# Performance work log

Hardware: AMD Instinct MI355X
Metric: run time of the kernel (lower is better)

## Reference

```python
import jax, jax.numpy as jnp
import numpy as np

K = 3
TAPS = K ** 3  # 27 taps of the 3x3x3 kernel


def _conv3d(x, w, b):
    # x: (B,C,T,H,W), w: (O,I,kT,kH,kW), stride 1, pad 1
    y = jax.lax.conv_general_dilated(
        x, w, window_strides=(1, 1, 1),
        padding=((1, 1), (1, 1), (1, 1)),
        dimension_numbers=('NCDHW', 'OIDHW', 'NCDHW'))
    return y + b[None, :, None, None, None]


def _bilinear(xt, ph, pw):
    # xt: (B,C,T,H,W) temporally-shifted features; ph/pw: (B,T,H,W) float coords
    # zero padding outside the spatial extent (matches deform-conv semantics)
    B, C, T, H, W = xt.shape
    h0 = jnp.floor(ph)
    w0 = jnp.floor(pw)
    lh = (ph - h0)[:, None]  # (B,1,T,H,W)
    lw = (pw - w0)[:, None]
    h0i = h0.astype(jnp.int32)
    w0i = w0.astype(jnp.int32)
    xf = xt.reshape(B, C, T, H * W)

    def gather(hi, wi):
        valid = (hi >= 0) & (hi < H) & (wi >= 0) & (wi < W)
        idx = (jnp.clip(hi, 0, H - 1) * W + jnp.clip(wi, 0, W - 1)).reshape(B, 1, T, H * W)
        v = jnp.take_along_axis(xf, jnp.broadcast_to(idx, (B, C, T, H * W)), axis=3)
        return v.reshape(B, C, T, H, W) * valid[:, None].astype(xt.dtype)

    v00 = gather(h0i, w0i)
    v01 = gather(h0i, w0i + 1)
    v10 = gather(h0i + 1, w0i)
    v11 = gather(h0i + 1, w0i + 1)
    return (v00 * (1 - lh) * (1 - lw) + v01 * (1 - lh) * lw
            + v10 * lh * (1 - lw) + v11 * lh * lw)


def _dcn_hw(x, w_off, b_off, w, b):
    # DeformConvPack_d with dimension='HW': offsets deform H/W only, temporal taps rigid
    B, C, T, H, W = x.shape
    off = _conv3d(x, w_off, b_off).reshape(B, TAPS, 2, T, H, W)  # (dy, dx) per tap
    x_pad = jnp.pad(x, ((0, 0), (0, 0), (1, 1), (0, 0), (0, 0)))  # zero pad T
    hh = jnp.arange(H, dtype=x.dtype)[None, None, :, None]
    ww = jnp.arange(W, dtype=x.dtype)[None, None, None, :]
    out = jnp.zeros((B, w.shape[0], T, H, W), x.dtype)
    k = 0
    for kt in range(K):
        xt = x_pad[:, :, kt:kt + T]  # rigid temporal shift for this tap
        for kh in range(K):
            for kw in range(K):
                ph = hh + (kh - 1) + off[:, k, 0]
                pw = ww + (kw - 1) + off[:, k, 1]
                s = _bilinear(xt, ph, pw)  # (B,C,T,H,W)
                out = out + jnp.einsum('bcthw,oc->bothw', s, w[:, :, kt, kh, kw])
                k += 1
    return out + b[None, :, None, None, None]


def setup_inputs() -> dict:
    key = jax.random.key(0)
    ks = jax.random.split(key, 9)
    nf, B, T, H, W = 64, 1, 7, 96, 96
    sc = 1.0 / np.sqrt(nf * TAPS)
    return {
        'x': jax.random.normal(ks[0], (B, nf, T, H, W), jnp.float32),
        'w_off0': jax.random.normal(ks[1], (2 * TAPS, nf, K, K, K), jnp.float32) * 0.01,
        'b_off0': jax.random.normal(ks[2], (2 * TAPS,), jnp.float32) * 0.01,
        'w0': jax.random.normal(ks[3], (nf, nf, K, K, K), jnp.float32) * sc,
        'b0': jax.random.normal(ks[4], (nf,), jnp.float32) * 0.01,
        'w_off1': jax.random.normal(ks[5], (2 * TAPS, nf, K, K, K), jnp.float32) * 0.01,
        'b_off1': jax.random.normal(ks[6], (2 * TAPS,), jnp.float32) * 0.01,
        'w1': jax.random.normal(ks[7], (nf, nf, K, K, K), jnp.float32) * sc,
        'b1': jax.random.normal(ks[8], (nf,), jnp.float32) * 0.01,
    }


def reference(x, w_off0, b_off0, w0, b0, w_off1, b_off1, w1, b1):
    y = _dcn_hw(x, w_off0, b_off0, w0, b0)
    y = jnp.where(y > 0, y, 0.1 * y)  # LeakyReLU(0.1)
    return _dcn_hw(y, w_off1, b_off1, w1, b1) + x
```

## Files before the change

kernel.cpp:

```cpp
#include <hip/hip_runtime.h>
#include <hip/hip_fp16.h>

#define T_DIM 7
#define H_DIM 96
#define W_DIM 96
#define HW    (H_DIM*W_DIM)
#define L_DIM (T_DIM*HW)
#define NTAPS 27

#define TR 8
#define TC 16
#define HR (TR+8)
#define HC (TC+8)
#define HROWB (HC*128)
#define HALO_B (HR*HROWB)
#define WBUF_OFF HALO_B
#define SOFF_OFF (HALO_B + 16384)
#define SOFF_STRIDE 108
#define SMEM_B (SOFF_OFF + 128*SOFF_STRIDE)

typedef __attribute__((ext_vector_type(8))) _Float16 f16x8;
typedef __attribute__((ext_vector_type(4))) float f32x4;

#define GLOAD16(gp, lp) \
    __builtin_amdgcn_global_load_lds((const __attribute__((address_space(1))) unsigned int*)(gp), \
                                     (__attribute__((address_space(3))) unsigned int*)(lp), 16, 0, 0)

__global__ void prep_weights(const float* __restrict__ woff0,
                             const float* __restrict__ w0,
                             const float* __restrict__ woff1,
                             const float* __restrict__ w1,
                             unsigned short* __restrict__ dst)
{
    int idx = blockIdx.x * 256 + threadIdx.x;
    const int per = NTAPS * 64 * 64;
    if (idx >= 4 * per) return;
    int which = idx / per;
    int r     = idx % per;
    int tap   = r / 4096;
    int o     = (r >> 6) & 63;
    int c     = r & 63;
    const float* src = (which == 0) ? woff0 : (which == 1) ? w0
                     : (which == 2) ? woff1 : w1;
    int omax = (which == 0 || which == 2) ? 54 : 64;
    float v = 0.f;
    if (o < omax) v = src[(o * 64 + c) * NTAPS + tap];
    __half h = __float2half(v);
    int slot = (((c >> 3) + o) & 7);
    int pos  = tap * 4096 + o * 64 + slot * 8 + (c & 7);
    dst[which * per + pos] = __half_as_ushort(h);
}

__global__ void transpose_x(const float* __restrict__ x, unsigned* __restrict__ xt2)
{
    __shared__ float tile[64][65];
    const int tid = threadIdx.x;
    const int lb  = blockIdx.x * 64;
    const int ln  = tid & 63;
    const int q   = tid >> 6;
#pragma unroll
    for (int i = 0; i < 16; ++i) {
        int c = q + 4 * i;
        tile[ln][c] = x[(size_t)c * L_DIM + lb + ln];
    }
    __syncthreads();
    const int ln2 = tid & 31, q2 = tid >> 5;
#pragma unroll
    for (int i = 0; i < 8; ++i) {
        int ll = q2 + 8 * i;
        __half2 h2 = __float22half2_rn(make_float2(tile[ll][2*ln2], tile[ll][2*ln2+1]));
        xt2[(size_t)(lb + ll) * 32 + ln2] = *reinterpret_cast<unsigned*>(&h2);
    }
}

#define STAGE_SLAB(KT) { \
    int tp_ = t + (KT) - 1; \
    int tps_ = min(max(tp_, 0), T_DIM - 1); \
    const unsigned char* sb_ = xb + (size_t)tps_ * HW * 128; \
    _Pragma("unroll") \
    for (int i = 0; i < 12; ++i) { \
        int p16_ = tid + i * 256; \
        int hr_ = p16_ / 192; \
        int rem_ = p16_ - hr_ * 192; \
        int hc_ = rem_ >> 3; \
        int sl_ = rem_ & 7; \
        int ch_ = (sl_ - hc_) & 7; \
        int gr_ = min(max(row0 - 4 + hr_, 0), H_DIM - 1); \
        int gc_ = min(max(col0 - 4 + hc_, 0), W_DIM - 1); \
        GLOAD16(sb_ + (size_t)(gr_ * W_DIM + gc_) * 128 + ch_ * 16, \
                smem + (i << 12) + (wv << 10)); \
    } }

#define WSTAGE(WG, K) { \
    const unsigned char* ws_ = (WG) + (size_t)(K) * 8192 + tid * 16; \
    unsigned char* ld_ = smem + WBUF_OFF + (((K) & 1) << 13) + (wv << 10); \
    GLOAD16(ws_,        ld_); \
    GLOAD16(ws_ + 4096, ld_ + 4096); }

#define READ_OFF(MT, K) ({ \
    unsigned u_ = *(const unsigned*)(smem + SOFF_OFF + \
        ((2 * wv + (MT)) * 16 + lr) * SOFF_STRIDE + (K) * 4); \
    __half22float2(*reinterpret_cast<__half2*>(&u_)); })

#define GATHER_D(MT, O2, A0, A1) { \
    float ph_ = (float)(row0 + 2 * wv + (MT) + kh - 1) + (O2).x; \
    float pw_ = (float)(col0 + lr + kw - 1) + (O2).y; \
    float hf_ = floorf(ph_), wf_ = floorf(pw_); \
    float lh_ = ph_ - hf_, lw_ = pw_ - wf_; \
    int h0_ = (int)hf_, w0_ = (int)wf_; \
    __align__(16) __half2 va_[8]; \
    const __half2 z2_ = __float2half2_rn(0.f); \
    _Pragma("unroll") \
    for (int p = 0; p < 8; ++p) va_[p] = z2_; \
    _Pragma("unroll") \
    for (int j = 0; j < 4; ++j) { \
        int hj_ = h0_ + (j >> 1), wj_ = w0_ + (j & 1); \
        bool v_ = tv && (hj_ >= 0) && (hj_ < H_DIM) && (wj_ >= 0) && (wj_ < W_DIM); \
        float wg_ = ((j >> 1) ? lh_ : 1.f - lh_) * ((j & 1) ? lw_ : 1.f - lw_); \
        __half2 cw_ = __float2half2_rn(v_ ? wg_ : 0.f); \
        int sr_ = min(max(hj_ - row0 + 4, 0), HR - 1); \
        int sc_ = min(max(wj_ - col0 + 4, 0), HC - 1); \
        const unsigned char* cell_ = smem + sr_ * HROWB + sc_ * 128; \
        f16x8 c0_ = *(const f16x8*)(cell_ + (((lk + sc_) & 7) << 4)); \
        f16x8 c1_ = *(const f16x8*)(cell_ + (((lk + 4 + sc_) & 7) << 4)); \
        const __half2* p0_ = (const __half2*)&c0_; \
        const __half2* p1_ = (const __half2*)&c1_; \
        _Pragma("unroll") \
        for (int d = 0; d < 4; ++d) { \
            va_[d]     = __hfma2(p0_[d], cw_, va_[d]); \
            va_[4 + d] = __hfma2(p1_[d], cw_, va_[4 + d]); \
        } \
    } \
    A0 = *reinterpret_cast<f16x8*>(&va_[0]); \
    A1 = *reinterpret_cast<f16x8*>(&va_[4]); }

#define GATHER_C(MT, A0, A1) { \
    int hj_ = row0 + 2 * wv + (MT) + kh - 1, wj_ = col0 + lr + kw - 1; \
    bool v_ = tv && (hj_ >= 0) && (hj_ < H_DIM) && (wj_ >= 0) && (wj_ < W_DIM); \
    int sr_ = 2 * wv + (MT) + kh + 3, sc_ = lr + kw + 3; \
    const unsigned char* cell_ = smem + sr_ * HROWB + sc_ * 128; \
    int4 z0_ = *(const int4*)(cell_ + (((lk + sc_) & 7) << 4)); \
    int4 z1_ = *(const int4*)(cell_ + (((lk + 4 + sc_) & 7) << 4)); \
    if (!v_) { z0_ = make_int4(0,0,0,0); z1_ = make_int4(0,0,0,0); } \
    A0 = *reinterpret_cast<f16x8*>(&z0_); \
    A1 = *reinterpret_cast<f16x8*>(&z1_); }

#define MFMA_F16(A, B, C) __builtin_amdgcn_mfma_f32_16x16x32_f16( \
    A, *reinterpret_cast<f16x8*>(&(B)), C, 0, 0, 0)

#define RUN_PHASE(DEF, WGBLP) { \
    const unsigned char* wgbl_ = (WGBLP); \
    asm volatile("s_waitcnt lgkmcnt(0)" ::: "memory"); \
    __builtin_amdgcn_s_barrier(); \
    STAGE_SLAB(0); \
    WSTAGE(wgbl_, 0); \
    float2 oc0, oc1, on0, on1; \
    oc0 = make_float2(0.f, 0.f); oc1 = oc0; on0 = oc0; on1 = oc0; \
    if (DEF) { oc0 = READ_OFF(0, 0); oc1 = READ_OFF(1, 0); } \
    asm volatile("s_waitcnt vmcnt(0)" ::: "memory"); \
    __builtin_amdgcn_s_barrier(); \
    __builtin_amdgcn_sched_barrier(0); \
    _Pragma("unroll 1") \
    for (int kt = 0; kt < 3; ++kt) { \
        if (kt > 0) { \
            asm volatile("s_waitcnt lgkmcnt(0)" ::: "memory"); \
            __builtin_amdgcn_s_barrier(); \
            STAGE_SLAB(kt); \
            asm volatile("s_waitcnt vmcnt(0)" ::: "memory"); \
            __builtin_amdgcn_s_barrier(); \
            __builtin_amdgcn_sched_barrier(0); \
        } \
        int tp = t + kt - 1; \
        bool tv = (tp >= 0) && (tp < T_DIM); \
        _Pragma("unroll 1") \
        for (int k9 = 0; k9 < 9; ++k9) { \
            int k = kt * 9 + k9; \
            if (k > 0) { \
                asm volatile("s_waitcnt vmcnt(0) lgkmcnt(0)" ::: "memory"); \
                __builtin_amdgcn_s_barrier(); \
                __builtin_amdgcn_sched_barrier(0); \
            } \
            if (k + 1 < NTAPS) { \
                WSTAGE(wgbl_, k + 1); \
                if (DEF) { on0 = READ_OFF(0, k + 1); on1 = READ_OFF(1, k + 1); } \
            } \
            int kh = k9 / 3, kw = k9 - (k9 / 3) * 3; \
            f16x8 a00, a01, a10, a11; \
            if (DEF) { GATHER_D(0, oc0, a00, a01); GATHER_D(1, oc1, a10, a11); } \
            else     { GATHER_C(0, a00, a01);      GATHER_C(1, a10, a11); } \
            const unsigned char* br_ = smem + WBUF_OFF + ((k & 1) << 13) + lr * 128; \
            _Pragma("unroll") \
            for (int n = 0; n < 4; ++n) { \
                f16x8 b0_ = *(const f16x8*)(br_ + n * 2048 + s0); \
                f16x8 b1_ = *(const f16x8*)(br_ + n * 2048 + s1); \
                acc[0][n] = MFMA_F16(a00, b0_, acc[0][n]); \
                acc[0][n] = MFMA_F16(a01, b1_, acc[0][n]); \
                acc[1][n] = MFMA_F16(a10, b0_, acc[1][n]); \
                acc[1][n] = MFMA_F16(a11, b1_, acc[1][n]); \
            } \
            oc0 = on0; oc1 = on1; \
        } \
    } }

template<int EPI>
__global__ __launch_bounds__(256, 2)
void dcn_m32(const unsigned short* __restrict__ xin,
             const unsigned short* __restrict__ Wtoff,
             const unsigned short* __restrict__ Wtm,
             const float* __restrict__ boff,
             const float* __restrict__ bmain,
             const float* __restrict__ resid,
             float* __restrict__ outf,
             unsigned short* __restrict__ outh)
{
    __shared__ __align__(16) unsigned char smem[SMEM_B];

    const int tid  = threadIdx.x;
    const int wv   = tid >> 6, lane = tid & 63;
    const int lr   = lane & 15, lk = lane >> 4;

    const int bid = blockIdx.x;
    const int wg  = (bid & 7) * 63 + (bid >> 3);
    const int t   = wg / 72;
    const int rg  = (wg % 72) / 6;
    const int cg  = wg % 6;
    const int row0 = rg * TR;
    const int col0 = cg * TC;

    const unsigned char* xb = (const unsigned char*)xin;

    const int s0 = ((lk + lr) & 7) << 4;
    const int s1 = ((lk + 4 + lr) & 7) << 4;

    f32x4 acc[2][4];
#pragma unroll
    for (int mt = 0; mt < 2; ++mt)
#pragma unroll
        for (int n = 0; n < 4; ++n) acc[mt][n] = (f32x4){0.f, 0.f, 0.f, 0.f};

    RUN_PHASE(false, (const unsigned char*)Wtoff);

#pragma unroll
    for (int n = 0; n < 4; ++n) {
        int o = n * 16 + lr;
        if (o < 54) {
            float bvA = boff[o];
#pragma unroll
            for (int mt = 0; mt < 2; ++mt)
#pragma unroll
                for (int i = 0; i < 4; ++i) {
                    int l = (2 * wv + mt) * 16 + lk * 4 + i;
                    float vv = acc[mt][n][i] + bvA;
                    *(unsigned short*)(smem + SOFF_OFF + l * SOFF_STRIDE + o * 2) =
                        __half_as_ushort(__float2half(vv));
                }
        }
    }
    __syncthreads();

#pragma unroll
    for (int mt = 0; mt < 2; ++mt)
#pragma unroll
        for (int n = 0; n < 4; ++n) acc[mt][n] = (f32x4){0.f, 0.f, 0.f, 0.f};

    RUN_PHASE(true, (const unsigned char*)Wtm);

    float bv[4];
#pragma unroll
    for (int n = 0; n < 4; ++n) bv[n] = bmain[n * 16 + lr];

    if (EPI == 1) {
#pragma unroll
        for (int mt = 0; mt < 2; ++mt) {
            size_t lrowmt = (size_t)t * HW + (size_t)(row0 + 2 * wv + mt) * W_DIM + col0;
#pragma unroll
            for (int n = 0; n < 4; ++n)
#pragma unroll
                for (int i = 0; i < 4; ++i) {
                    int lc = lk * 4 + i;
                    float vv = acc[mt][n][i] + bv[n];
                    vv = (vv > 0.f) ? vv : 0.1f * vv;
                    outh[(lrowmt + lc) * 64 + n * 16 + lr] =
                        __half_as_ushort(__float2half(vv));
                }
        }
    } else {
        __syncthreads();
        float* tf = (float*)(smem + (wv << 13));
#pragma unroll
        for (int mt = 0; mt < 2; ++mt)
#pragma unroll
            for (int n = 0; n < 4; ++n)
#pragma unroll
                for (int i = 0; i < 4; ++i) {
                    int l = mt * 16 + lk * 4 + i;
                    int och = n * 16 + lr;
                    tf[l * 64 + ((och + 2 * l) & 63)] = acc[mt][n][i] + bv[n];
                }
        asm volatile("s_waitcnt lgkmcnt(0)" ::: "memory");
        __builtin_amdgcn_sched_barrier(0);
        int j = lane & 15, gq = lane >> 4;
#pragma unroll
        for (int mt = 0; mt < 2; ++mt) {
            size_t lrowmt = (size_t)t * HW + (size_t)(row0 + 2 * wv + mt) * W_DIM + col0;
#pragma unroll
            for (int it = 0; it < 16; ++it) {
                int och = gq * 16 + it;
                int l = mt * 16 + j;
                float val = tf[l * 64 + ((och + 2 * l) & 63)];
                size_t gi = (size_t)och * L_DIM + lrowmt + j;
                outf[gi] = val + resid[gi];
            }
        }
    }
}

extern "C" void kernel_launch(void* const* d_in, const int* in_sizes, int n_in,
                              void* d_out, int out_size, void* d_ws, size_t ws_size,
                              hipStream_t stream)
{
    const float* x     = (const float*)d_in[0];
    const float* woff0 = (const float*)d_in[1];
    const float* boff0 = (const float*)d_in[2];
    const float* w0    = (const float*)d_in[3];
    const float* b0    = (const float*)d_in[4];
    const float* woff1 = (const float*)d_in[5];
    const float* boff1 = (const float*)d_in[6];
    const float* w1    = (const float*)d_in[7];
    const float* b1    = (const float*)d_in[8];
    float* out = (float*)d_out;

    unsigned char* ws = (unsigned char*)d_ws;
    unsigned short* Wt  = (unsigned short*)ws;
    unsigned short* xt  = (unsigned short*)(ws + 884736);
    unsigned short* y   = (unsigned short*)(ws + 9142272);

    prep_weights<<<1728, 256, 0, stream>>>(woff0, w0, woff1, w1, Wt);
    transpose_x<<<1008, 256, 0, stream>>>(x, (unsigned*)xt);

    const int grid = T_DIM * (H_DIM / TR) * (W_DIM / TC);
    const int WSZ  = NTAPS * 64 * 64;

    dcn_m32<1><<<grid, 256, 0, stream>>>(xt, Wt,           Wt + WSZ,     boff0, b0, nullptr, nullptr, y);
    dcn_m32<2><<<grid, 256, 0, stream>>>(y,  Wt + 2 * WSZ, Wt + 3 * WSZ, boff1, b1, x, out, nullptr);
}
```

Baseline: 129.9 us.

## Stage zero-padded halo so bilinear gather drops per-corner validity checks

Halo staging now loads from a zero buffer for out-of-range spatial or temporal positions, so the shared slab already contains the zero padding. The deformable gather then computes one clamped base cell, reads the four corners as two adjacent rows and columns, and blends them with a fixed mul/fma chain with no per-corner validity masking. The rigid gather also drops its mask. This trims ALU and branch work in the hot gather loop. The cost is an extra tiny zero-fill kernel launch, and samples whose offsets fall beyond the halo are clamped to edge cells, which differs from exact zero-pad semantics.

```diff
diff --git a/kernel.cpp b/kernel.cpp
--- a/kernel.cpp
+++ b/kernel.cpp
@@ -25,6 +25,11 @@
 #define GLOAD16(gp, lp) \
     __builtin_amdgcn_global_load_lds((const __attribute__((address_space(1))) unsigned int*)(gp), \
                                      (__attribute__((address_space(3))) unsigned int*)(lp), 16, 0, 0)
+
+__global__ void zfill(int4* __restrict__ z)
+{
+    z[threadIdx.x] = make_int4(0, 0, 0, 0);
+}
 
 __global__ void prep_weights(const float* __restrict__ woff0,
                              const float* __restrict__ w0,
@@ -75,8 +80,8 @@
 
 #define STAGE_SLAB(KT) { \
     int tp_ = t + (KT) - 1; \
-    int tps_ = min(max(tp_, 0), T_DIM - 1); \
-    const unsigned char* sb_ = xb + (size_t)tps_ * HW * 128; \
+    bool tvz_ = (tp_ >= 0) && (tp_ < T_DIM); \
+    const unsigned char* sb_ = xb + (size_t)(tvz_ ? tp_ : 0) * HW * 128; \
     _Pragma("unroll") \
     for (int i = 0; i < 12; ++i) { \
         int p16_ = tid + i * 256; \
@@ -85,10 +90,13 @@
         int hc_ = rem_ >> 3; \
         int sl_ = rem_ & 7; \
         int ch_ = (sl_ - hc_) & 7; \
-        int gr_ = min(max(row0 - 4 + hr_, 0), H_DIM - 1); \
-        int gc_ = min(max(col0 - 4 + hc_, 0), W_DIM - 1); \
-        GLOAD16(sb_ + (size_t)(gr_ * W_DIM + gc_) * 128 + ch_ * 16, \
-                smem + (i << 12) + (wv << 10)); \
+        int gr_ = row0 - 4 + hr_; \
+        int gc_ = col0 - 4 + hc_; \
+        bool ok_ = tvz_ && (gr_ >= 0) && (gr_ < H_DIM) && (gc_ >= 0) && (gc_ < W_DIM); \
+        const unsigned char* src_ = ok_ \
+            ? (sb_ + (size_t)(gr_ * W_DIM + gc_) * 128 + ch_ * 16) \
+            : (zb + sl_ * 16); \
+        GLOAD16(src_, smem + (i << 12) + (wv << 10)); \
     } }
 
 #define WSTAGE(WG, K) { \
@@ -107,41 +115,52 @@
     float pw_ = (float)(col0 + lr + kw - 1) + (O2).y; \
     float hf_ = floorf(ph_), wf_ = floorf(pw_); \
     float lh_ = ph_ - hf_, lw_ = pw_ - wf_; \
-    int h0_ = (int)hf_, w0_ = (int)wf_; \
+    int sr_ = min(max((int)hf_ - row0 + 4, 0), HR - 2); \
+    int sc_ = min(max((int)wf_ - col0 + 4, 0), HC - 2); \
+    __half2 cw00_ = __float2half2_rn((1.f - lh_) * (1.f - lw_)); \
+    __half2 cw01_ = __float2half2_rn((1.f - lh_) * lw_); \
+    __half2 cw10_ = __float2half2_rn(lh_ * (1.f - lw_)); \
+    __half2 cw11_ = __float2half2_rn(lh_ * lw_); \
+    const unsigned char* r0_ = smem + sr_ * HROWB; \
+    const unsigned char* r1_ = r0_ + HROWB; \
+    int c0a_ = sc_ * 128 + (((lk + sc_) & 7) << 4); \
+    int c0b_ = sc_ * 128 + (((lk + 4 + sc_) & 7) << 4); \
+    int c1a_ = (sc_ + 1) * 128 + (((lk + 1 + sc_) & 7) << 4); \
+    int c1b_ = (sc_ + 1) * 128 + (((lk + 5 + sc_) & 7) << 4); \
+    f16x8 v00a_ = *(const f16x8*)(r0_ + c0a_), v00b_ = *(const f16x8*)(r0_ + c0b_); \
+    f16x8 v01a_ = *(const f16x8*)(r0_ + c1a_), v01b_ = *(const f16x8*)(r0_ + c1b_); \
+    f16x8 v10a_ = *(const f16x8*)(r1_ + c0a_), v10b_ = *(const f16x8*)(r1_ + c0b_); \
+    f16x8 v11a_ = *(const f16x8*)(r1_ + c1a_), v11b_ = *(const f16x8*)(r1_ + c1b_); \
     __align__(16) __half2 va_[8]; \
-    const __half2 z2_ = __float2half2_rn(0.f); \
+    const __half2* p00a_ = (const __half2*)&v00a_; \
+    const __half2* p01a_ = (const __half2*)&v01a_; \
+    const __half2* p10a_ = (const __half2*)&v10a_; \
+    const __half2* p11a_ = (const __half2*)&v11a_; \
+    const __half2* p00b_ = (const __half2*)&v00b_; \
+    const __half2* p01b_ = (const __half2*)&v01b_; \
+    const __half2* p10b_ = (const __half2*)&v10b_; \
+    const __half2* p11b_ = (const __half2*)&v11b_; \
     _Pragma("unroll") \
-    for (int p = 0; p < 8; ++p) va_[p] = z2_; \
-    _Pragma("unroll") \
-    for (int j = 0; j < 4; ++j) { \
-        int hj_ = h0_ + (j >> 1), wj_ = w0_ + (j & 1); \
-        bool v_ = tv && (hj_ >= 0) && (hj_ < H_DIM) && (wj_ >= 0) && (wj_ < W_DIM); \
-        float wg_ = ((j >> 1) ? lh_ : 1.f - lh_) * ((j & 1) ? lw_ : 1.f - lw_); \
-        __half2 cw_ = __float2half2_rn(v_ ? wg_ : 0.f); \
-        int sr_ = min(max(hj_ - row0 + 4, 0), HR - 1); \
-        int sc_ = min(max(wj_ - col0 + 4, 0), HC - 1); \
-        const unsigned char* cell_ = smem + sr_ * HROWB + sc_ * 128; \
-        f16x8 c0_ = *(const f16x8*)(cell_ + (((lk + sc_) & 7) << 4)); \
-        f16x8 c1_ = *(const f16x8*)(cell_ + (((lk + 4 + sc_) & 7) << 4)); \
-        const __half2* p0_ = (const __half2*)&c0_; \
-        const __half2* p1_ = (const __half2*)&c1_; \
-        _Pragma("unroll") \
-        for (int d = 0; d < 4; ++d) { \
-            va_[d]     = __hfma2(p0_[d], cw_, va_[d]); \
-            va_[4 + d] = __hfma2(p1_[d], cw_, va_[4 + d]); \
-        } \
+    for (int d = 0; d < 4; ++d) { \
+        __half2 s0_ = __hmul2(p00a_[d], cw00_); \
+        s0_ = __hfma2(p01a_[d], cw01_, s0_); \
+        s0_ = __hfma2(p10a_[d], cw10_, s0_); \
+        s0_ = __hfma2(p11a_[d], cw11_, s0_); \
+        va_[d] = s0_; \
+        __half2 s1_ = __hmul2(p00b_[d], cw00_); \
+        s1_ = __hfma2(p01b_[d], cw01_, s1_); \
+        s1_ = __hfma2(p10b_[d], cw10_, s1_); \
+        s1_ = __hfma2(p11b_[d], cw11_, s1_); \
+        va_[4 + d] = s1_; \
     } \
     A0 = *reinterpret_cast<f16x8*>(&va_[0]); \
     A1 = *reinterpret_cast<f16x8*>(&va_[4]); }
 
 #define GATHER_C(MT, A0, A1) { \
-    int hj_ = row0 + 2 * wv + (MT) + kh - 1, wj_ = col0 + lr + kw - 1; \
-    bool v_ = tv && (hj_ >= 0) && (hj_ < H_DIM) && (wj_ >= 0) && (wj_ < W_DIM); \
     int sr_ = 2 * wv + (MT) + kh + 3, sc_ = lr + kw + 3; \
     const unsigned char* cell_ = smem + sr_ * HROWB + sc_ * 128; \
     int4 z0_ = *(const int4*)(cell_ + (((lk + sc_) & 7) << 4)); \
     int4 z1_ = *(const int4*)(cell_ + (((lk + 4 + sc_) & 7) << 4)); \
-    if (!v_) { z0_ = make_int4(0,0,0,0); z1_ = make_int4(0,0,0,0); } \
     A0 = *reinterpret_cast<f16x8*>(&z0_); \
     A1 = *reinterpret_cast<f16x8*>(&z1_); }
 
@@ -170,8 +189,6 @@
             __builtin_amdgcn_s_barrier(); \
             __builtin_amdgcn_sched_barrier(0); \
         } \
-        int tp = t + kt - 1; \
-        bool tv = (tp >= 0) && (tp < T_DIM); \
         _Pragma("unroll 1") \
         for (int k9 = 0; k9 < 9; ++k9) { \
             int k = kt * 9 + k9; \
@@ -204,14 +221,15 @@
 
 template<int EPI>
 __global__ __launch_bounds__(256, 2)
-void dcn_m32(const unsigned short* __restrict__ xin,
-             const unsigned short* __restrict__ Wtoff,
-             const unsigned short* __restrict__ Wtm,
-             const float* __restrict__ boff,
-             const float* __restrict__ bmain,
-             const float* __restrict__ resid,
-             float* __restrict__ outf,
-             unsigned short* __restrict__ outh)
+void dcn_zp(const unsigned short* __restrict__ xin,
+            const unsigned short* __restrict__ Wtoff,
+            const unsigned short* __restrict__ Wtm,
+            const float* __restrict__ boff,
+            const float* __restrict__ bmain,
+            const float* __restrict__ resid,
+            const unsigned char* __restrict__ zb,
+            float* __restrict__ outf,
+            unsigned short* __restrict__ outh)
 {
     __shared__ __align__(16) unsigned char smem[SMEM_B];
 
@@ -334,13 +352,15 @@
     unsigned short* Wt  = (unsigned short*)ws;
     unsigned short* xt  = (unsigned short*)(ws + 884736);
     unsigned short* y   = (unsigned short*)(ws + 9142272);
-
+    unsigned char*  zb  = ws + 17399808;
+
+    zfill<<<1, 256, 0, stream>>>((int4*)zb);
     prep_weights<<<1728, 256, 0, stream>>>(woff0, w0, woff1, w1, Wt);
     transpose_x<<<1008, 256, 0, stream>>>(x, (unsigned*)xt);
 
     const int grid = T_DIM * (H_DIM / TR) * (W_DIM / TC);
     const int WSZ  = NTAPS * 64 * 64;
 
-    dcn_m32<1><<<grid, 256, 0, stream>>>(xt, Wt,           Wt + WSZ,     boff0, b0, nullptr, nullptr, y);
-    dcn_m32<2><<<grid, 256, 0, stream>>>(y,  Wt + 2 * WSZ, Wt + 3 * WSZ, boff1, b1, x, out, nullptr);
-}
+    dcn_zp<1><<<grid, 256, 0, stream>>>(xt, Wt,           Wt + WSZ,     boff0, b0, nullptr, zb, nullptr, y);
+    dcn_zp<2><<<grid, 256, 0, stream>>>(y,  Wt + 2 * WSZ, Wt + 3 * WSZ, boff1, b1, x,       zb, out, nullptr);
+}
```

Result: no change. 128.6 us (median of 2 runs) (-1.0%).
